# Kernel tuning notes

Hardware: AMD Instinct MI355X
Metric: run time of the kernel (lower is better)

## Reference

```python
import jax, jax.numpy as jnp
import numpy as np

B, N, E, D, R = 32, 2048, 8192, 512, 8
V_SENSE = 25000
V_GLOBAL = 50000  # last_idx_globals - last_idx_senses


def setup_inputs() -> dict:
    key = jax.random.key(0)
    ks = jax.random.split(key, 12)
    x = jax.random.normal(ks[0], (B, N, D), dtype=jnp.float32)
    edge_index = jax.random.randint(ks[1], (B, 2, E), 0, N)
    edge_type = jax.random.randint(ks[2], (B, E), 0, R)
    s = 0.02
    basis = jax.random.normal(ks[3], (R, D, D), dtype=jnp.float32) * s   # num_bases = R
    comp = jax.random.normal(ks[4], (R, R), dtype=jnp.float32) * s      # [num_relations, num_bases]
    root = jax.random.normal(ks[5], (D, D), dtype=jnp.float32) * s
    bias_conv = jnp.zeros((D,), dtype=jnp.float32)
    w_global = jax.random.normal(ks[6], (V_GLOBAL, D), dtype=jnp.float32) * s
    b_global = jnp.zeros((V_GLOBAL,), dtype=jnp.float32)
    w_sense = jax.random.normal(ks[7], (V_SENSE, D), dtype=jnp.float32) * s
    b_sense = jnp.zeros((V_SENSE,), dtype=jnp.float32)
    return {"x": x, "edge_index": edge_index, "edge_type": edge_type,
            "basis": basis, "comp": comp, "root": root, "bias_conv": bias_conv,
            "w_global": w_global, "b_global": b_global,
            "w_sense": w_sense, "b_sense": b_sense}


def reference(x, edge_index, edge_type, basis, comp, root, bias_conv,
              w_global, b_global, w_sense, b_sense):
    # Basis decomposition: per-relation weight W_r = sum_b comp[r,b] * basis[b]
    W = jnp.einsum('rb,bio->rio', comp, basis)  # [R, D, D]

    def conv_one(xg, ei, et):
        # RGCNConv with mean aggregation per relation + root transform + bias
        src, dst = ei[0], ei[1]
        x_src = xg[src]                              # [E, D] gather
        out = xg @ root + bias_conv                  # [N, D]
        for r in range(R):                           # fixed small relation loop
            mask = (et == r).astype(xg.dtype)        # [E]
            msg = (x_src @ W[r]) * mask[:, None]     # [E, D]
            s = jax.ops.segment_sum(msg, dst, num_segments=N)              # [N, D]
            cnt = jax.ops.segment_sum(mask, dst, num_segments=N)           # [N]
            out = out + s / jnp.maximum(cnt, 1.0)[:, None]                 # mean aggr
        return out

    h = jax.vmap(conv_one)(x, edge_index, edge_type)  # [B, N, D]
    h = jax.nn.relu(h)
    h0 = h[:, 0]                                      # current node per sample [B, D]
    logits_global = h0 @ w_global.T + b_global        # [B, V_GLOBAL]
    logits_sense = h0 @ w_sense.T + b_sense           # [B, V_SENSE]
    return (jax.nn.log_softmax(logits_global, axis=-1),
            jax.nn.log_softmax(logits_sense, axis=-1))
```

## Files before the change

kernel.cpp:

```cpp
#include <hip/hip_runtime.h>
#include <hip/hip_bf16.h>

#define BATCH 32
#define NNODE 2048
#define NEDGE 8192
#define DIM   512
#define NREL  8
#define VG    50000
#define VS    25000
#define ZI    4608
#define NCH   36
#define NT_G  3125
#define NT_S  1563
#define TTOT  4688
#define NBLK8 1172

typedef __attribute__((ext_vector_type(4))) float f32x4;
typedef __attribute__((ext_vector_type(8))) short s16x8;

__global__ __launch_bounds__(512) void k_conv(const float* __restrict__ x,
                                              const int* __restrict__ ei,
                                              const int* __restrict__ et,
                                              const float* __restrict__ comp,
                                              float* __restrict__ z) {
    int g = blockIdx.x;
    int t = threadIdx.x;
    int wv = t >> 6, lane = t & 63;
    __shared__ int elds[8 * 128];
    __shared__ int wcnt[8];
    const int* srcp = ei + (size_t)(g * 2 + 0) * NEDGE;
    const int* dstp = ei + (size_t)(g * 2 + 1) * NEDGE;

    int run = 0;
    for (int it = 0; it < 16; it++) {
        int e = wv * 1024 + it * 64 + lane;
        bool m = (dstp[e] == 0);
        unsigned long long mask = __ballot(m);
        int rank = __popcll(mask & ((1ull << lane) - 1ull));
        if (m && (run + rank) < 128) elds[wv * 128 + run + rank] = e;
        run += (int)__popcll(mask);
    }
    if (lane == 0) wcnt[wv] = (run > 128) ? 128 : run;
    __syncthreads();

    int d = t;
    float s0=0,s1=0,s2=0,s3=0,s4=0,s5=0,s6=0,s7=0;
    int   c0=0,c1=0,c2=0,c3=0,c4=0,c5=0,c6=0,c7=0;
    for (int w = 0; w < 8; w++) {
        int cw = wcnt[w];
        for (int i = 0; i < cw; i++) {
            int e = elds[w * 128 + i];
            int r = et[(size_t)g * NEDGE + e];
            int sn = srcp[e];
            float val = x[((size_t)g * NNODE + sn) * DIM + d];
            if (r == 0) { s0 += val; c0++; }
            if (r == 1) { s1 += val; c1++; }
            if (r == 2) { s2 += val; c2++; }
            if (r == 3) { s3 += val; c3++; }
            if (r == 4) { s4 += val; c4++; }
            if (r == 5) { s5 += val; c5++; }
            if (r == 6) { s6 += val; c6++; }
            if (r == 7) { s7 += val; c7++; }
        }
    }
    float sv[8] = {s0,s1,s2,s3,s4,s5,s6,s7};
    float inv[8];
    int   cv[8] = {c0,c1,c2,c3,c4,c5,c6,c7};
    #pragma unroll
    for (int r = 0; r < 8; r++) inv[r] = 1.0f / fmaxf((float)cv[r], 1.0f);

    z[(size_t)g * ZI + d] = x[((size_t)g * NNODE + 0) * DIM + d];
    #pragma unroll
    for (int b = 0; b < 8; b++) {
        float y = 0.f;
        #pragma unroll
        for (int r = 0; r < 8; r++) y += comp[r * 8 + b] * inv[r] * sv[r];
        z[(size_t)g * ZI + 512 + b * 512 + d] = y;
    }
}

__global__ __launch_bounds__(512) void k_gemm_part(const float* __restrict__ z,
                                                   const float* __restrict__ root,
                                                   const float* __restrict__ basis,
                                                   float* __restrict__ part2) {
    int bx = blockIdx.x;
    int dt = bx & 3;
    int cc = bx >> 2;
    int t = threadIdx.x;
    int dl = t & 127, gq = t >> 7;
    __shared__ float ztT[128][33];
    #pragma unroll
    for (int rep = 0; rep < 8; rep++) {
        int flat = rep * 512 + t;
        int g = flat >> 7, i = flat & 127;
        ztT[i][g] = z[(size_t)g * ZI + cc * 128 + i];
    }
    __syncthreads();
    const float* M = (cc < 4) ? (root + (size_t)(cc * 128) * 512)
                              : (basis + (size_t)((cc - 4) * 128) * 512);
    float acc[8] = {0,0,0,0,0,0,0,0};
    for (int i = 0; i < 128; i++) {
        float m = M[(size_t)i * 512 + dt * 128 + dl];
        #pragma unroll
        for (int j = 0; j < 8; j++) acc[j] += ztT[i][gq * 8 + j] * m;
    }
    #pragma unroll
    for (int j = 0; j < 8; j++) {
        int g = gq * 8 + j;
        part2[((size_t)cc * 32 + g) * 512 + dt * 128 + dl] = acc[j];
    }
}

__device__ __forceinline__ unsigned bf16rne(float f) {
    unsigned u = __float_as_uint(f);
    return (u + 0x7FFFu + ((u >> 16) & 1u)) >> 16;
}

__global__ __launch_bounds__(256) void k_h0(const float* __restrict__ part2,
                                            const float* __restrict__ bias_conv,
                                            unsigned* __restrict__ h0t) {
    int g = blockIdx.x;
    int p = threadIdx.x;
    int d0 = 2 * p;
    float v0 = bias_conv[d0], v1 = bias_conv[d0 + 1];
    for (int cc = 0; cc < NCH; cc++) {
        const float* pp = part2 + ((size_t)cc * 32 + g) * 512 + d0;
        v0 += pp[0];
        v1 += pp[1];
    }
    v0 = fmaxf(v0, 0.f);
    v1 = fmaxf(v1, 0.f);
    h0t[g * 256 + p] = bf16rne(v0) | (bf16rne(v1) << 16);
}

__device__ __forceinline__ short f2bf(float f) {
    __hip_bfloat16 h = __float2bfloat16(f);
    return *reinterpret_cast<short*>(&h);
}

__global__ __launch_bounds__(256, 4) void k_logits8(const unsigned* __restrict__ h0t,
                                                    const float* __restrict__ wg,
                                                    const float* __restrict__ bg,
                                                    const float* __restrict__ wsn,
                                                    const float* __restrict__ bsv,
                                                    float* __restrict__ out,
                                                    float* __restrict__ part) {
    __shared__ __align__(16) unsigned char hlds[32768];

    int t = threadIdx.x;
    int wv = t >> 6, l = t & 63;

    #pragma unroll
    for (int rep = 0; rep < 8; rep++) {
        int idx = rep * 256 + t;
        int g = idx >> 6, q = idx & 63;
        uint4 val = *(const uint4*)&h0t[idx * 4];
        *(uint4*)&hlds[g * 1024 + ((q ^ (g & 7)) << 4)] = val;
    }
    __syncthreads();

    int tile = blockIdx.x * 4 + wv;
    const float* w; const float* bias; float* ob; int V; int v0;
    if (tile < NT_G) { w = wg;  bias = bg;  ob = out;                      V = VG; v0 = tile * 16; }
    else             { w = wsn; bias = bsv; ob = out + (size_t)BATCH * VG; V = VS; v0 = (tile - NT_G) * 16; }

    int c  = l & 15;
    int kg = l >> 4;
    int vb = v0 + c;
    int vr = (vb < V) ? vb : (V - 1);
    const f32x4* __restrict__ wrow = (const f32x4*)(w + (size_t)vr * 512) + kg * 2;
    int swz = c & 7;
    const unsigned char* ha = &hlds[c * 1024];
    const unsigned char* hb = &hlds[(c + 16) * 1024];

    f32x4 wb[4][2];
    #pragma unroll
    for (int p = 0; p < 4; p++) {
        wb[p][0] = __builtin_nontemporal_load(&wrow[p * 8]);
        wb[p][1] = __builtin_nontemporal_load(&wrow[p * 8 + 1]);
    }

    f32x4 acc0 = {0.f, 0.f, 0.f, 0.f};
    f32x4 acc1 = {0.f, 0.f, 0.f, 0.f};

    #pragma unroll
    for (int kc = 0; kc < 16; kc++) {
        f32x4 b0 = wb[kc & 3][0];
        f32x4 b1 = wb[kc & 3][1];
        if (kc + 4 < 16) {
            wb[kc & 3][0] = __builtin_nontemporal_load(&wrow[(kc + 4) * 8]);
            wb[kc & 3][1] = __builtin_nontemporal_load(&wrow[(kc + 4) * 8 + 1]);
        }
        int gr = ((kc * 4 + kg) ^ swz) << 4;
        s16x8 a0 = *(const s16x8*)(ha + gr);
        s16x8 a1 = *(const s16x8*)(hb + gr);
        s16x8 bf;
        bf[0] = f2bf(b0[0]); bf[1] = f2bf(b0[1]); bf[2] = f2bf(b0[2]); bf[3] = f2bf(b0[3]);
        bf[4] = f2bf(b1[0]); bf[5] = f2bf(b1[1]); bf[6] = f2bf(b1[2]); bf[7] = f2bf(b1[3]);
        acc0 = __builtin_amdgcn_mfma_f32_16x16x32_bf16(a0, bf, acc0, 0, 0, 0);
        acc1 = __builtin_amdgcn_mfma_f32_16x16x32_bf16(a1, bf, acc1, 0, 0, 0);
    }

    float p0[4], p1[4];
    bool valid = (vb < V);
    float bia = valid ? bias[vb] : 0.f;
    #pragma unroll
    for (int j = 0; j < 4; j++) {
        float v0f = acc0[j] + bia;
        float v1f = acc1[j] + bia;
        int g0 = kg * 4 + j;
        if (valid) {
            ob[(size_t)g0 * V + vb]        = v0f;
            ob[(size_t)(g0 + 16) * V + vb] = v1f;
        }
        p0[j] = valid ? __expf(v0f) : 0.f;
        p1[j] = valid ? __expf(v1f) : 0.f;
    }
    #pragma unroll
    for (int s = 1; s < 16; s <<= 1) {
        #pragma unroll
        for (int j = 0; j < 4; j++) {
            p0[j] += __shfl_xor(p0[j], s);
            p1[j] += __shfl_xor(p1[j], s);
        }
    }
    if (c == 0) {
        float* pt = part + (size_t)tile * 32;
        #pragma unroll
        for (int j = 0; j < 4; j++) {
            pt[kg * 4 + j]      = p0[j];
            pt[kg * 4 + j + 16] = p1[j];
        }
    }
}

__global__ __launch_bounds__(256) void k_lse64(const float* __restrict__ part,
                                               float* __restrict__ lse) {
    int bx = blockIdx.x;
    int head = bx >> 5, g = bx & 31;
    int tbase = head ? NT_G : 0;
    int ntl   = head ? (TTOT - NT_G) : NT_G;
    int t = threadIdx.x;
    float s = 0.f;
    for (int i = t; i < ntl; i += 256)
        s += part[(size_t)(tbase + i) * 32 + g];
    #pragma unroll
    for (int m = 1; m < 64; m <<= 1) s += __shfl_xor(s, m);
    __shared__ float ws4[4];
    if ((t & 63) == 0) ws4[t >> 6] = s;
    __syncthreads();
    if (t == 0) lse[bx] = logf(ws4[0] + ws4[1] + ws4[2] + ws4[3]);
}

__global__ __launch_bounds__(256) void k_sub(float* __restrict__ out,
                                             const float* __restrict__ lse) {
    unsigned i4 = blockIdx.x * 256u + threadIdx.x;
    if (i4 >= 600000u) return;
    unsigned idx = i4 * 4u;
    float l;
    if (idx < 1600000u) l = lse[idx / 50000u];
    else                l = lse[32u + (idx - 1600000u) / 25000u];
    float4 v = *(float4*)(out + idx);
    v.x -= l; v.y -= l; v.z -= l; v.w -= l;
    *(float4*)(out + idx) = v;
}

extern "C" void kernel_launch(void* const* d_in, const int* in_sizes, int n_in,
                              void* d_out, int out_size, void* d_ws, size_t ws_size,
                              hipStream_t stream) {
    const float* x        = (const float*)d_in[0];
    const int*   ei       = (const int*)  d_in[1];
    const int*   et       = (const int*)  d_in[2];
    const float* basis    = (const float*)d_in[3];
    const float* comp     = (const float*)d_in[4];
    const float* root     = (const float*)d_in[5];
    const float* biasc    = (const float*)d_in[6];
    const float* wg       = (const float*)d_in[7];
    const float* bg       = (const float*)d_in[8];
    const float* wsn      = (const float*)d_in[9];
    const float* bsv      = (const float*)d_in[10];
    float* out = (float*)d_out;

    float* z     = out;
    float* part2 = out + (size_t)BATCH * ZI;
    unsigned* h0t  = (unsigned*)d_ws;
    float*    part = (float*)d_ws + 8192;
    float*    lse  = part + (size_t)TTOT * 32;

    k_conv     <<<BATCH, 512, 0, stream>>>(x, ei, et, comp, z);
    k_gemm_part<<<NCH * 4, 512, 0, stream>>>(z, root, basis, part2);
    k_h0       <<<BATCH, 256, 0, stream>>>(part2, biasc, h0t);
    k_logits8  <<<NBLK8, 256, 0, stream>>>(h0t, wg, bg, wsn, bsv, out, part);
    k_lse64    <<<64, 256, 0, stream>>>(part, lse);
    k_sub      <<<2344, 256, 0, stream>>>(out, lse);
}
```

Measured before the change: 78.24 us.

## Stream vocab weights into LDS via async global_load_lds with double-buffered tiles

Replaces the logits kernel with single-wave blocks that each handle two 16-row vocab tiles. Weight rows are copied into LDS with global_load_lds, double-buffered across K halves and tiles, with manual vmcnt waits. The bf16 hidden states are kept in registers and used as the B operand. The aim is to overlap the weight stream, the memory-bound part, with MFMA compute and to avoid register-staged loads, at the cost of heavy register use for h0 and reliance on hand-counted waitcnts.

```diff
diff --git a/kernel.cpp b/kernel.cpp
--- a/kernel.cpp
+++ b/kernel.cpp
@@ -11,9 +11,10 @@
 #define ZI    4608
 #define NCH   36
 #define NT_G  3125
-#define NT_S  1563
 #define TTOT  4688
-#define NBLK8 1172
+#define NW9   2344
+#define ROWB  1040
+#define BUFB  16640
 
 typedef __attribute__((ext_vector_type(4))) float f32x4;
 typedef __attribute__((ext_vector_type(8))) short s16x8;
@@ -133,105 +134,134 @@
     h0t[g * 256 + p] = bf16rne(v0) | (bf16rne(v1) << 16);
 }
 
+__device__ __forceinline__ void gload_lds16(const float* gsrc, float* ldst) {
+    __builtin_amdgcn_global_load_lds(
+        (const __attribute__((address_space(1))) void*)gsrc,
+        (__attribute__((address_space(3))) void*)ldst,
+        16, 0, 0);
+}
+
 __device__ __forceinline__ short f2bf(float f) {
     __hip_bfloat16 h = __float2bfloat16(f);
     return *reinterpret_cast<short*>(&h);
 }
 
-__global__ __launch_bounds__(256, 4) void k_logits8(const unsigned* __restrict__ h0t,
-                                                    const float* __restrict__ wg,
-                                                    const float* __restrict__ bg,
-                                                    const float* __restrict__ wsn,
-                                                    const float* __restrict__ bsv,
-                                                    float* __restrict__ out,
-                                                    float* __restrict__ part) {
-    __shared__ __align__(16) unsigned char hlds[32768];
-
-    int t = threadIdx.x;
-    int wv = t >> 6, l = t & 63;
-
-    #pragma unroll
-    for (int rep = 0; rep < 8; rep++) {
-        int idx = rep * 256 + t;
-        int g = idx >> 6, q = idx & 63;
-        uint4 val = *(const uint4*)&h0t[idx * 4];
-        *(uint4*)&hlds[g * 1024 + ((q ^ (g & 7)) << 4)] = val;
-    }
-    __syncthreads();
-
-    int tile = blockIdx.x * 4 + wv;
-    const float* w; const float* bias; float* ob; int V; int v0;
-    if (tile < NT_G) { w = wg;  bias = bg;  ob = out;                      V = VG; v0 = tile * 16; }
-    else             { w = wsn; bias = bsv; ob = out + (size_t)BATCH * VG; V = VS; v0 = (tile - NT_G) * 16; }
-
-    int c  = l & 15;
-    int kg = l >> 4;
-    int vb = v0 + c;
-    int vr = (vb < V) ? vb : (V - 1);
-    const f32x4* __restrict__ wrow = (const f32x4*)(w + (size_t)vr * 512) + kg * 2;
-    int swz = c & 7;
-    const unsigned char* ha = &hlds[c * 1024];
-    const unsigned char* hb = &hlds[(c + 16) * 1024];
-
-    f32x4 wb[4][2];
-    #pragma unroll
-    for (int p = 0; p < 4; p++) {
-        wb[p][0] = __builtin_nontemporal_load(&wrow[p * 8]);
-        wb[p][1] = __builtin_nontemporal_load(&wrow[p * 8 + 1]);
-    }
-
-    f32x4 acc0 = {0.f, 0.f, 0.f, 0.f};
-    f32x4 acc1 = {0.f, 0.f, 0.f, 0.f};
-
-    #pragma unroll
-    for (int kc = 0; kc < 16; kc++) {
-        f32x4 b0 = wb[kc & 3][0];
-        f32x4 b1 = wb[kc & 3][1];
-        if (kc + 4 < 16) {
-            wb[kc & 3][0] = __builtin_nontemporal_load(&wrow[(kc + 4) * 8]);
-            wb[kc & 3][1] = __builtin_nontemporal_load(&wrow[(kc + 4) * 8 + 1]);
+#define VMWAIT(n) asm volatile("s_waitcnt vmcnt(" #n ")" ::: "memory")
+#define MEMFENCE() asm volatile("" ::: "memory")
+
+__global__ __launch_bounds__(64) void k_logits9(const unsigned* __restrict__ h0t,
+                                                const float* __restrict__ wg,
+                                                const float* __restrict__ bg,
+                                                const float* __restrict__ wsn,
+                                                const float* __restrict__ bsv,
+                                                float* __restrict__ out,
+                                                float* __restrict__ part) {
+    __shared__ __align__(16) unsigned char wlds[2 * BUFB];
+
+    int l = threadIdx.x;
+    int w = blockIdx.x;
+    int t0 = w, t1 = w + NW9;
+
+    const float *w0p, *b0p, *w1p, *b1p;
+    float *o0p, *o1p;
+    int V0, V1, v00, v01;
+    if (t0 < NT_G) { w0p = wg;  b0p = bg;  o0p = out;                      V0 = VG; v00 = t0 * 16; }
+    else           { w0p = wsn; b0p = bsv; o0p = out + (size_t)BATCH * VG; V0 = VS; v00 = (t0 - NT_G) * 16; }
+    if (t1 < NT_G) { w1p = wg;  b1p = bg;  o1p = out;                      V1 = VG; v01 = t1 * 16; }
+    else           { w1p = wsn; b1p = bsv; o1p = out + (size_t)BATCH * VG; V1 = VS; v01 = (t1 - NT_G) * 16; }
+
+    int vrow = (l >> 4) * 4;
+    float bA[4], bB[4];
+    #pragma unroll
+    for (int j = 0; j < 4; j++) {
+        int va = v00 + vrow + j;  bA[j] = b0p[va < V0 ? va : V0 - 1];
+        int vb = v01 + vrow + j;  bB[j] = b1p[vb < V1 ? vb : V1 - 1];
+    }
+    s16x8 h0f[16][2];
+    {
+        const unsigned char* hbase = (const unsigned char*)h0t;
+        int hoff = (l & 15) * 1024 + (l >> 4) * 16;
+        #pragma unroll
+        for (int kc = 0; kc < 16; kc++) {
+            h0f[kc][0] = *(const s16x8*)(hbase + hoff + kc * 64);
+            h0f[kc][1] = *(const s16x8*)(hbase + 16384 + hoff + kc * 64);
         }
-        int gr = ((kc * 4 + kg) ^ swz) << 4;
-        s16x8 a0 = *(const s16x8*)(ha + gr);
-        s16x8 a1 = *(const s16x8*)(hb + gr);
-        s16x8 bf;
-        bf[0] = f2bf(b0[0]); bf[1] = f2bf(b0[1]); bf[2] = f2bf(b0[2]); bf[3] = f2bf(b0[3]);
-        bf[4] = f2bf(b1[0]); bf[5] = f2bf(b1[1]); bf[6] = f2bf(b1[2]); bf[7] = f2bf(b1[3]);
-        acc0 = __builtin_amdgcn_mfma_f32_16x16x32_bf16(a0, bf, acc0, 0, 0, 0);
-        acc1 = __builtin_amdgcn_mfma_f32_16x16x32_bf16(a1, bf, acc1, 0, 0, 0);
-    }
-
-    float p0[4], p1[4];
-    bool valid = (vb < V);
-    float bia = valid ? bias[vb] : 0.f;
-    #pragma unroll
-    for (int j = 0; j < 4; j++) {
-        float v0f = acc0[j] + bia;
-        float v1f = acc1[j] + bia;
-        int g0 = kg * 4 + j;
-        if (valid) {
-            ob[(size_t)g0 * V + vb]        = v0f;
-            ob[(size_t)(g0 + 16) * V + vb] = v1f;
-        }
-        p0[j] = valid ? __expf(v0f) : 0.f;
-        p1[j] = valid ? __expf(v1f) : 0.f;
-    }
-    #pragma unroll
-    for (int s = 1; s < 16; s <<= 1) {
-        #pragma unroll
-        for (int j = 0; j < 4; j++) {
-            p0[j] += __shfl_xor(p0[j], s);
-            p1[j] += __shfl_xor(p1[j], s);
-        }
-    }
-    if (c == 0) {
-        float* pt = part + (size_t)tile * 32;
-        #pragma unroll
-        for (int j = 0; j < 4; j++) {
-            pt[kg * 4 + j]      = p0[j];
-            pt[kg * 4 + j + 16] = p1[j];
-        }
-    }
+    }
+    MEMFENCE();
+
+#define ISSUE(WP, V0_, VLIM, BUF, KH) do {                                    \
+        _Pragma("unroll")                                                     \
+        for (int r = 0; r < 16; r++) {                                        \
+            int vr = (V0_) + r; if (vr > (VLIM) - 1) vr = (VLIM) - 1;         \
+            const float* srcp = (WP) + (size_t)vr * 512 + (KH) * 256 + l * 4; \
+            gload_lds16(srcp, (float*)&wlds[(BUF) * BUFB + r * ROWB]);        \
+        }                                                                     \
+    } while (0)
+
+#define COMPUTE(KH, BUF, A0, A1) do {                                         \
+        const unsigned char* wbp = wlds + (BUF) * BUFB + (l & 15) * ROWB      \
+                                   + ((l >> 4) * 32);                         \
+        _Pragma("unroll")                                                     \
+        for (int kcl = 0; kcl < 8; kcl++) {                                   \
+            f32x4 wlo = *(const f32x4*)(wbp + kcl * 128);                     \
+            f32x4 whi = *(const f32x4*)(wbp + kcl * 128 + 16);                \
+            s16x8 a;                                                          \
+            a[0] = f2bf(wlo[0]); a[1] = f2bf(wlo[1]);                         \
+            a[2] = f2bf(wlo[2]); a[3] = f2bf(wlo[3]);                         \
+            a[4] = f2bf(whi[0]); a[5] = f2bf(whi[1]);                         \
+            a[6] = f2bf(whi[2]); a[7] = f2bf(whi[3]);                         \
+            A0 = __builtin_amdgcn_mfma_f32_16x16x32_bf16(a, h0f[(KH)*8+kcl][0], A0, 0, 0, 0); \
+            A1 = __builtin_amdgcn_mfma_f32_16x16x32_bf16(a, h0f[(KH)*8+kcl][1], A1, 0, 0, 0); \
+        }                                                                     \
+    } while (0)
+
+#define STORE(TIL, OP, VLIM, V0_, BP4, A0, A1) do {                           \
+        float s0 = 0.f, s1 = 0.f;                                             \
+        _Pragma("unroll")                                                     \
+        for (int j = 0; j < 4; j++) {                                         \
+            int v = (V0_) + vrow + j;                                         \
+            float L0 = A0[j] + BP4[j];                                        \
+            float L1 = A1[j] + BP4[j];                                        \
+            if (v < (VLIM)) {                                                 \
+                (OP)[(size_t)(l & 15) * (VLIM) + v]        = L0;              \
+                (OP)[(size_t)(16 + (l & 15)) * (VLIM) + v] = L1;              \
+                s0 += __expf(L0);                                             \
+                s1 += __expf(L1);                                             \
+            }                                                                 \
+        }                                                                     \
+        s0 += __shfl_xor(s0, 16); s0 += __shfl_xor(s0, 32);                   \
+        s1 += __shfl_xor(s1, 16); s1 += __shfl_xor(s1, 32);                   \
+        if (l < 16) {                                                         \
+            part[(size_t)(TIL) * 32 + l]      = s0;                           \
+            part[(size_t)(TIL) * 32 + 16 + l] = s1;                           \
+        }                                                                     \
+    } while (0)
+
+    f32x4 accA0 = {0.f,0.f,0.f,0.f}, accA1 = {0.f,0.f,0.f,0.f};
+    f32x4 accB0 = {0.f,0.f,0.f,0.f}, accB1 = {0.f,0.f,0.f,0.f};
+
+    ISSUE(w0p, v00, V0, 0, 0);
+    ISSUE(w0p, v00, V0, 1, 1);
+
+    VMWAIT(16);
+    COMPUTE(0, 0, accA0, accA1);
+    ISSUE(w1p, v01, V1, 0, 0);
+
+    VMWAIT(16);
+    COMPUTE(1, 1, accA0, accA1);
+    ISSUE(w1p, v01, V1, 1, 1);
+
+    VMWAIT(16);
+    STORE(t0, o0p, V0, v00, bA, accA0, accA1);
+    COMPUTE(0, 0, accB0, accB1);
+
+    VMWAIT(0);
+    COMPUTE(1, 1, accB0, accB1);
+    STORE(t1, o1p, V1, v01, bB, accB0, accB1);
+
+#undef ISSUE
+#undef COMPUTE
+#undef STORE
 }
 
 __global__ __launch_bounds__(256) void k_lse64(const float* __restrict__ part,
@@ -290,7 +320,7 @@
     k_conv     <<<BATCH, 512, 0, stream>>>(x, ei, et, comp, z);
     k_gemm_part<<<NCH * 4, 512, 0, stream>>>(z, root, basis, part2);
     k_h0       <<<BATCH, 256, 0, stream>>>(part2, biasc, h0t);
-    k_logits8  <<<NBLK8, 256, 0, stream>>>(h0t, wg, bg, wsn, bsv, out, part);
+    k_logits9  <<<NW9, 64, 0, stream>>>(h0t, wg, bg, wsn, bsv, out, part);
     k_lse64    <<<64, 256, 0, stream>>>(part, lse);
     k_sub      <<<2344, 256, 0, stream>>>(out, lse);
 }
```

New measurement: 80.15 us. 1.02x slower.
